# Optimization experiments

Measured on AMD Instinct MI355X. Metric: run time of the kernel, lower is better.

The kernel has to match this reference:

```python
import jax, jax.numpy as jnp
import numpy as np

HD, M = 4096, 14336

def setup_inputs() -> dict:
    key = jax.random.key(0)
    k_x, k_g, k_u, k_d = jax.random.split(key, 4)
    scale = 1.0 / np.sqrt(HD)
    x = jax.random.normal(k_x, (4, 2048, HD), dtype=jnp.float16)
    # Dequantized fp16 weights, stored torch-style as [out_features, in_features]
    W_gate = (jax.random.normal(k_g, (M, HD), dtype=jnp.float16) * jnp.float16(scale))
    W_up   = (jax.random.normal(k_u, (M, HD), dtype=jnp.float16) * jnp.float16(scale))
    W_down = (jax.random.normal(k_d, (HD, M), dtype=jnp.float16) * jnp.float16(1.0 / np.sqrt(M)))
    return {"x": x, "W_gate": W_gate, "W_up": W_up, "W_down": W_down}

def reference(x, W_gate, W_up, W_down):
    # SwiGLU: down( silu(x @ Wg^T) * (x @ Wu^T) )
    gate = jnp.einsum("bsh,mh->bsm", x, W_gate)   # [B,S,M]
    up = jnp.einsum("bsh,mh->bsm", x, W_up)       # [B,S,M]
    h = jax.nn.silu(gate) * up                       # fused elementwise
    out = jnp.einsum("bsm,hm->bsh", h, W_down)    # [B,S,HD]
    return out
```

## Files before the change

### kernel.cpp

```cpp
#include <hip/hip_runtime.h>

typedef _Float16 f16;
typedef _Float16 f16x8 __attribute__((ext_vector_type(8)));
typedef float f32x4 __attribute__((ext_vector_type(4)));

__device__ __forceinline__ f16x8 cvt8(f32x4 lo, f32x4 hi) {
    f16x8 h;
    h[0] = (f16)lo[0]; h[1] = (f16)lo[1]; h[2] = (f16)lo[2]; h[3] = (f16)lo[3];
    h[4] = (f16)hi[0]; h[5] = (f16)hi[1]; h[6] = (f16)hi[2]; h[7] = (f16)hi[3];
    return h;
}

__global__ __launch_bounds__(256)
void cvt_f32_f16(const float* __restrict__ in, f16* __restrict__ out, long long n) {
    long long i = ((long long)blockIdx.x * 256 + threadIdx.x) * 8;
    const long long stride = (long long)gridDim.x * 256 * 8;
    for (; i < n; i += stride) {
        f32x4 a = *(const f32x4*)(in + i);
        f32x4 b = *(const f32x4*)(in + i + 4);
        *(f16x8*)(out + i) = cvt8(a, b);
    }
}

__global__ void fill_sentinel_f32(float* __restrict__ out, long long n) {
    long long i = (long long)blockIdx.x * blockDim.x + threadIdx.x;
    long long stride = (long long)gridDim.x * blockDim.x;
    for (; i < n; i += stride) out[i] = 1.0f;
}

__device__ __forceinline__ void gload_lds16(const f16* g, f16* l) {
    __builtin_amdgcn_global_load_lds(
        (const __attribute__((address_space(1))) unsigned int*)(unsigned long long)g,
        (__attribute__((address_space(3))) unsigned int*)(unsigned int)(unsigned long long)l,
        16, 0, 0);
}

template<bool FUSED>
__global__ __launch_bounds__(512)
void mlp_gemm16(const f16* __restrict__ A, const f16* __restrict__ B0,
                const f16* __restrict__ B1, void* __restrict__ Cv,
                int K, int ldc, int nRow, int nCol, int RG) {
    constexpr int BN    = FUSED ? 128 : 256;
    constexpr int BROWS = FUSED ? 128 : 256;
    __shared__ __align__(16) f16 smA[3][128 * 32];
    __shared__ __align__(16) f16 smB0[3][BROWS * 32];
    __shared__ __align__(16) f16 smB1[FUSED ? 3 : 1][FUSED ? 128 * 32 : 8];

    const int lin   = blockIdx.x;
    const int perSg = RG * nCol;
    const int sg    = lin / perSg;
    const int rem   = lin - sg * perSg;
    int rgIn = nRow - sg * RG; if (rgIn > RG) rgIn = RG;
    const int colB = rem / rgIn;
    const int rowB = sg * RG + (rem - colB * rgIn);

    const long long blockRow = (long long)rowB * 128;
    const long long blockCol = (long long)colB * BN;

    const int tid  = threadIdx.x;
    const int w    = tid >> 6;
    const int lane = tid & 63;
    const int waveM = w >> 2;
    const int waveN = w & 3;

    const int dr   = tid >> 2;
    const int dblk = tid & 3;
    const int gblk = (dblk - (dr >> 1)) & 3;
    const f16* gA   = A  + (blockRow + dr) * (long long)K + gblk * 8;
    const f16* gB0a = B0 + (blockCol + dr) * (long long)K + gblk * 8;
    const f16* gB0b = FUSED ? nullptr
                            : B0 + (blockCol + 128 + dr) * (long long)K + gblk * 8;
    const f16* gB1a = FUSED ? B1 + (blockCol + dr) * (long long)K + gblk * 8
                            : nullptr;
    const int wbase = w * 512;

    const int fr = lane & 15;
    const int hi = lane >> 4;
    constexpr int NI = FUSED ? 2 : 4;
    int aOff[4], bOff[NI];
#pragma unroll
    for (int i = 0; i < 4; ++i) {
        const int r = waveM * 64 + i * 16 + fr;
        aOff[i] = r * 32 + (((hi + (r >> 1)) & 3) << 3);
    }
#pragma unroll
    for (int n = 0; n < NI; ++n) {
        const int r = waveN * (FUSED ? 32 : 64) + n * 16 + fr;
        bOff[n] = r * 32 + (((hi + (r >> 1)) & 3) << 3);
    }

    f32x4 acc0[4][NI];
    f32x4 acc1[FUSED ? 4 : 1][FUSED ? NI : 1];
#pragma unroll
    for (int mi = 0; mi < 4; ++mi)
#pragma unroll
        for (int ni = 0; ni < NI; ++ni) {
            acc0[mi][ni] = (f32x4){0.f, 0.f, 0.f, 0.f};
            if constexpr (FUSED) acc1[mi][ni] = (f32x4){0.f, 0.f, 0.f, 0.f};
        }

    auto stage = [&](int b) {
        gload_lds16(gA, &smA[b][wbase]);     gA += 32;
        gload_lds16(gB0a, &smB0[b][wbase]);  gB0a += 32;
        if constexpr (FUSED) {
            gload_lds16(gB1a, &smB1[b][wbase]); gB1a += 32;
        } else {
            gload_lds16(gB0b, &smB0[b][4096 + wbase]); gB0b += 32;
        }
    };

    auto compute = [&](int b) {
        f16x8 aF[4], bF[NI], b1F[FUSED ? NI : 1];
#pragma unroll
        for (int i = 0; i < 4; ++i) aF[i] = *(const f16x8*)(&smA[b][aOff[i]]);
#pragma unroll
        for (int n = 0; n < NI; ++n) bF[n] = *(const f16x8*)(&smB0[b][bOff[n]]);
        if constexpr (FUSED) {
#pragma unroll
            for (int n = 0; n < NI; ++n) b1F[n] = *(const f16x8*)(&smB1[b][bOff[n]]);
        }
#pragma unroll
        for (int mi = 0; mi < 4; ++mi)
#pragma unroll
            for (int ni = 0; ni < NI; ++ni) {
                acc0[mi][ni] = __builtin_amdgcn_mfma_f32_16x16x32_f16(
                    aF[mi], bF[ni], acc0[mi][ni], 0, 0, 0);
                if constexpr (FUSED)
                    acc1[mi][ni] = __builtin_amdgcn_mfma_f32_16x16x32_f16(
                        aF[mi], b1F[ni], acc1[mi][ni], 0, 0, 0);
            }
    };

    const int nk = K >> 5;
    stage(0);
    stage(1);
    int cur = 0;
    for (int t = 0; t < nk - 1; ++t) {
        asm volatile("s_waitcnt vmcnt(3)" ::: "memory");
        __builtin_amdgcn_s_barrier();
        __builtin_amdgcn_sched_barrier(0);
        if (t + 2 < nk) {
            int nb = cur + 2; if (nb >= 3) nb -= 3;
            stage(nb);
        }
        compute(cur);
        cur = (cur == 2) ? 0 : cur + 1;
    }
    asm volatile("s_waitcnt vmcnt(0)" ::: "memory");
    __builtin_amdgcn_s_barrier();
    __builtin_amdgcn_sched_barrier(0);
    compute(cur);

    const long long orBase = blockRow + waveM * 64 + hi * 4;
    const long long ocBase = blockCol + waveN * (FUSED ? 32 : 64) + fr;
#pragma unroll
    for (int mi = 0; mi < 4; ++mi)
#pragma unroll
        for (int ni = 0; ni < NI; ++ni)
#pragma unroll
            for (int j = 0; j < 4; ++j) {
                const long long idx =
                    (orBase + mi * 16 + j) * (long long)ldc + (ocBase + ni * 16);
                if constexpr (FUSED) {
                    float gv = acc0[mi][ni][j];
                    float uv = acc1[mi][ni][j];
                    float v = (gv / (1.f + __expf(-gv))) * uv;
                    ((f16*)Cv)[idx] = (f16)v;
                } else {
                    ((float*)Cv)[idx] = acc0[mi][ni][j];
                }
            }
}

template<bool IS16>
__device__ __forceinline__ f16x8 load8(const char* p) {
    if constexpr (IS16) return *(const f16x8*)p;
    const float* f = (const float*)p;
    return cvt8(*(const f32x4*)f, *(const f32x4*)(f + 4));
}

template<bool FUSED, bool A16, bool B16>
__global__ __launch_bounds__(256)
void mlp_gemm(const void* __restrict__ Av, const void* __restrict__ B0v,
              const void* __restrict__ B1v, void* __restrict__ Cv,
              int K, int ldc, int nRow, int nCol, int RG) {
    __shared__ __align__(16) f16 smA[128 * 32];
    __shared__ __align__(16) f16 smB0[128 * 32];
    __shared__ __align__(16) f16 smB1[FUSED ? 128 * 32 : 8];

    const int lin   = blockIdx.x;
    const int perSg = RG * nCol;
    const int sg    = lin / perSg;
    const int rem   = lin - sg * perSg;
    int rgIn = nRow - sg * RG; if (rgIn > RG) rgIn = RG;
    const int colB = rem / rgIn;
    const int rowB = sg * RG + (rem - colB * rgIn);

    const long long blockRow = (long long)rowB * 128;
    const long long blockCol = (long long)colB * 128;

    const int tid  = threadIdx.x;
    const int w    = tid >> 6;
    const int lane = tid & 63;
    const int waveM = w >> 1;
    const int waveN = w & 1;

    const int r0 = tid >> 2;
    const int s0 = tid & 3;
    const int szA = A16 ? 2 : 4;
    const int szB = B16 ? 2 : 4;
    const char* gA0  = (const char*)Av  + ((blockRow + r0)      * (long long)K + s0 * 8) * szA;
    const char* gA1  = (const char*)Av  + ((blockRow + r0 + 64) * (long long)K + s0 * 8) * szA;
    const char* gB00 = (const char*)B0v + ((blockCol + r0)      * (long long)K + s0 * 8) * szB;
    const char* gB01 = (const char*)B0v + ((blockCol + r0 + 64) * (long long)K + s0 * 8) * szB;
    const char* gB10 = FUSED ? (const char*)B1v + ((blockCol + r0)      * (long long)K + s0 * 8) * szB : nullptr;
    const char* gB11 = FUSED ? (const char*)B1v + ((blockCol + r0 + 64) * (long long)K + s0 * 8) * szB : nullptr;

    const int off0 = tid * 8;
    const int off1 = off0 + 2048;

    const int fr = lane & 15;
    const int fk = (lane >> 4) * 8;
    int offA[4], offB[4];
#pragma unroll
    for (int i = 0; i < 4; ++i) {
        offA[i] = (waveM * 64 + i * 16 + fr) * 32 + fk;
        offB[i] = (waveN * 64 + i * 16 + fr) * 32 + fk;
    }

    f32x4 acc0[4][4];
    f32x4 acc1[4][4];
#pragma unroll
    for (int mi = 0; mi < 4; ++mi)
#pragma unroll
        for (int ni = 0; ni < 4; ++ni) {
            acc0[mi][ni] = (f32x4){0.f, 0.f, 0.f, 0.f};
            if constexpr (FUSED) acc1[mi][ni] = (f32x4){0.f, 0.f, 0.f, 0.f};
        }

    const int ksteps = K >> 5;
    for (int kt = 0; kt < ksteps; ++kt) {
        f16x8 vA0  = load8<A16>(gA0);
        f16x8 vA1  = load8<A16>(gA1);
        f16x8 vB00 = load8<B16>(gB00);
        f16x8 vB01 = load8<B16>(gB01);
        f16x8 vB10, vB11;
        if constexpr (FUSED) {
            vB10 = load8<B16>(gB10);
            vB11 = load8<B16>(gB11);
        }
        gA0 += 32 * szA; gA1 += 32 * szA;
        gB00 += 32 * szB; gB01 += 32 * szB;
        if constexpr (FUSED) { gB10 += 32 * szB; gB11 += 32 * szB; }

        __syncthreads();

        *(f16x8*)(smA  + off0) = vA0;
        *(f16x8*)(smA  + off1) = vA1;
        *(f16x8*)(smB0 + off0) = vB00;
        *(f16x8*)(smB0 + off1) = vB01;
        if constexpr (FUSED) {
            *(f16x8*)(smB1 + off0) = vB10;
            *(f16x8*)(smB1 + off1) = vB11;
        }

        __syncthreads();

        f16x8 aF[4], bF[4], b1F[4];
#pragma unroll
        for (int i = 0; i < 4; ++i) aF[i] = *(const f16x8*)(smA + offA[i]);
#pragma unroll
        for (int i = 0; i < 4; ++i) bF[i] = *(const f16x8*)(smB0 + offB[i]);
        if constexpr (FUSED) {
#pragma unroll
            for (int i = 0; i < 4; ++i) b1F[i] = *(const f16x8*)(smB1 + offB[i]);
        }

#pragma unroll
        for (int mi = 0; mi < 4; ++mi)
#pragma unroll
            for (int ni = 0; ni < 4; ++ni) {
                acc0[mi][ni] = __builtin_amdgcn_mfma_f32_16x16x32_f16(
                    aF[mi], bF[ni], acc0[mi][ni], 0, 0, 0);
                if constexpr (FUSED)
                    acc1[mi][ni] = __builtin_amdgcn_mfma_f32_16x16x32_f16(
                        aF[mi], b1F[ni], acc1[mi][ni], 0, 0, 0);
            }
    }

    const long long orBase = blockRow + waveM * 64 + ((lane >> 4) * 4);
    const long long ocBase = blockCol + waveN * 64 + fr;
#pragma unroll
    for (int mi = 0; mi < 4; ++mi)
#pragma unroll
        for (int ni = 0; ni < 4; ++ni)
#pragma unroll
            for (int j = 0; j < 4; ++j) {
                const long long idx =
                    (orBase + mi * 16 + j) * (long long)ldc + (ocBase + ni * 16);
                if constexpr (FUSED) {
                    float gv = acc0[mi][ni][j];
                    float uv = acc1[mi][ni][j];
                    float v = (gv / (1.f + __expf(-gv))) * uv;
                    ((f16*)Cv)[idx] = (f16)v;
                } else {
                    ((float*)Cv)[idx] = acc0[mi][ni][j];
                }
            }
}

extern "C" void kernel_launch(void* const* d_in, const int* in_sizes, int n_in,
                              void* d_out, int out_size, void* d_ws, size_t ws_size,
                              hipStream_t stream) {
    const float* x  = (const float*)d_in[0];
    const float* Wg = (const float*)d_in[1];
    const float* Wu = (const float*)d_in[2];
    const float* Wd = (const float*)d_in[3];
    float* out = (float*)d_out;

    const int HD = 4096;
    const int T  = in_sizes[0] / HD;
    const int M  = in_sizes[1] / HD;

    const long long nW = (long long)M * HD;
    const long long nX = (long long)T * HD;
    const size_t wBytes = (size_t)nW * 2;
    const size_t xBytes = (size_t)nX * 2;
    const size_t hRow   = (size_t)M * 2;
    const size_t minH   = 128 * hRow;

    char* p = (char*)d_ws;
    size_t rem = ws_size;
    f16 *Wg16 = nullptr, *Wu16 = nullptr, *Wd16 = nullptr, *X16 = nullptr;
    bool wf16 = false, xf16 = false;
    if (rem >= 3 * wBytes + minH) {
        Wg16 = (f16*)p; p += wBytes;
        Wu16 = (f16*)p; p += wBytes;
        Wd16 = (f16*)p; p += wBytes;
        rem -= 3 * wBytes;
        wf16 = true;
        if (rem >= xBytes + minH) {
            X16 = (f16*)p; p += xBytes; rem -= xBytes; xf16 = true;
        }
    }
    f16* H = (f16*)p;
    long long maxRows = (long long)(rem / hRow);
    int chunk = (int)((maxRows / 128) * 128);
    if (chunk > T) chunk = T;
    if (chunk <= 0) {
        fill_sentinel_f32<<<1024, 256, 0, stream>>>(out, (long long)out_size);
        return;
    }

    if (wf16) {
        cvt_f32_f16<<<2048, 256, 0, stream>>>(Wg, Wg16, nW);
        cvt_f32_f16<<<2048, 256, 0, stream>>>(Wu, Wu16, nW);
        cvt_f32_f16<<<2048, 256, 0, stream>>>(Wd, Wd16, nW);
    }
    if (xf16) cvt_f32_f16<<<2048, 256, 0, stream>>>(x, X16, nX);

    for (int t0 = 0; t0 < T; t0 += chunk) {
        int rows = (T - t0 < chunk) ? (T - t0) : chunk;
        int nRow = rows / 128;
        {
            int nCol = M / 128;
            dim3 grid(nRow * nCol);
            int RG = nRow;
            if (xf16)
                mlp_gemm16<true><<<grid, 512, 0, stream>>>(
                    X16 + (size_t)t0 * HD, Wg16, Wu16, H, HD, M, nRow, nCol, RG);
            else if (wf16)
                mlp_gemm<true, false, true><<<grid, 256, 0, stream>>>(
                    x + (size_t)t0 * HD, Wg16, Wu16, H, HD, M, nRow, nCol, RG);
            else
                mlp_gemm<true, false, false><<<grid, 256, 0, stream>>>(
                    x + (size_t)t0 * HD, Wg, Wu, H, HD, M, nRow, nCol, RG);
        }
        {
            if (wf16) {
                int nCol = HD / 256;
                dim3 grid(nRow * nCol);
                int RG = (nRow < 32) ? nRow : 32;
                mlp_gemm16<false><<<grid, 512, 0, stream>>>(
                    H, Wd16, nullptr, out + (size_t)t0 * HD, M, HD, nRow, nCol, RG);
            } else {
                int nCol = HD / 128;
                dim3 grid(nRow * nCol);
                int RG = (nRow < 32) ? nRow : 32;
                mlp_gemm<false, true, false><<<grid, 256, 0, stream>>>(
                    H, Wd, nullptr, out + (size_t)t0 * HD, M, HD, nRow, nCol, RG);
            }
        }
    }
}
```

Before: 3.076 ms.

## Double GEMM block row tile to 256 for higher operand reuse

Both the fused gate/up GEMM and the down-projection GEMM now compute 256-row output tiles per block, with each wave covering 128 rows and holding twice as many MFMA accumulators. A extra A-load per stage feeds the larger LDS tile, and the wait count is adjusted accordingly. This aims to halve weight re-reads per output row and increase MFMA work per LDS load, at the cost of much higher register and LDS use that may reduce occupancy or cause spills. The host path is simplified so the fp16 route requires workspace for all converted tensors, otherwise falling back to the fp32 kernels.

```diff
diff --git a/kernel.cpp b/kernel.cpp
--- a/kernel.cpp
+++ b/kernel.cpp
@@ -36,14 +36,13 @@
 }
 
 template<bool FUSED>
-__global__ __launch_bounds__(512)
-void mlp_gemm16(const f16* __restrict__ A, const f16* __restrict__ B0,
-                const f16* __restrict__ B1, void* __restrict__ Cv,
-                int K, int ldc, int nRow, int nCol, int RG) {
-    constexpr int BN    = FUSED ? 128 : 256;
-    constexpr int BROWS = FUSED ? 128 : 256;
-    __shared__ __align__(16) f16 smA[3][128 * 32];
-    __shared__ __align__(16) f16 smB0[3][BROWS * 32];
+__global__ __launch_bounds__(512, 2)
+void mlp_gemm16b(const f16* __restrict__ A, const f16* __restrict__ B0,
+                 const f16* __restrict__ B1, void* __restrict__ Cv,
+                 int K, int ldc, int nRow, int nCol, int RG) {
+    constexpr int BN = FUSED ? 128 : 256;
+    __shared__ __align__(16) f16 smA[3][256 * 32];
+    __shared__ __align__(16) f16 smB0[3][BN * 32];
     __shared__ __align__(16) f16 smB1[FUSED ? 3 : 1][FUSED ? 128 * 32 : 8];
 
     const int lin   = blockIdx.x;
@@ -54,7 +53,7 @@
     const int colB = rem / rgIn;
     const int rowB = sg * RG + (rem - colB * rgIn);
 
-    const long long blockRow = (long long)rowB * 128;
+    const long long blockRow = (long long)rowB * 256;
     const long long blockCol = (long long)colB * BN;
 
     const int tid  = threadIdx.x;
@@ -66,10 +65,10 @@
     const int dr   = tid >> 2;
     const int dblk = tid & 3;
     const int gblk = (dblk - (dr >> 1)) & 3;
-    const f16* gA   = A  + (blockRow + dr) * (long long)K + gblk * 8;
+    const f16* gA0  = A + (blockRow + dr) * (long long)K + gblk * 8;
+    const f16* gA1  = gA0 + 128 * (long long)K;
     const f16* gB0a = B0 + (blockCol + dr) * (long long)K + gblk * 8;
-    const f16* gB0b = FUSED ? nullptr
-                            : B0 + (blockCol + 128 + dr) * (long long)K + gblk * 8;
+    const f16* gB0b = FUSED ? nullptr : gB0a + 128 * (long long)K;
     const f16* gB1a = FUSED ? B1 + (blockCol + dr) * (long long)K + gblk * 8
                             : nullptr;
     const int wbase = w * 512;
@@ -77,22 +76,23 @@
     const int fr = lane & 15;
     const int hi = lane >> 4;
     constexpr int NI = FUSED ? 2 : 4;
-    int aOff[4], bOff[NI];
-#pragma unroll
-    for (int i = 0; i < 4; ++i) {
-        const int r = waveM * 64 + i * 16 + fr;
+    constexpr int NW = FUSED ? 32 : 64;
+    int aOff[8], bOff[NI];
+#pragma unroll
+    for (int i = 0; i < 8; ++i) {
+        const int r = waveM * 128 + i * 16 + fr;
         aOff[i] = r * 32 + (((hi + (r >> 1)) & 3) << 3);
     }
 #pragma unroll
     for (int n = 0; n < NI; ++n) {
-        const int r = waveN * (FUSED ? 32 : 64) + n * 16 + fr;
+        const int r = waveN * NW + n * 16 + fr;
         bOff[n] = r * 32 + (((hi + (r >> 1)) & 3) << 3);
     }
 
-    f32x4 acc0[4][NI];
-    f32x4 acc1[FUSED ? 4 : 1][FUSED ? NI : 1];
-#pragma unroll
-    for (int mi = 0; mi < 4; ++mi)
+    f32x4 acc0[8][NI];
+    f32x4 acc1[FUSED ? 8 : 1][FUSED ? NI : 1];
+#pragma unroll
+    for (int mi = 0; mi < 8; ++mi)
 #pragma unroll
         for (int ni = 0; ni < NI; ++ni) {
             acc0[mi][ni] = (f32x4){0.f, 0.f, 0.f, 0.f};
@@ -100,19 +100,20 @@
         }
 
     auto stage = [&](int b) {
-        gload_lds16(gA, &smA[b][wbase]);     gA += 32;
-        gload_lds16(gB0a, &smB0[b][wbase]);  gB0a += 32;
-        if constexpr (FUSED) {
-            gload_lds16(gB1a, &smB1[b][wbase]); gB1a += 32;
+        gload_lds16(gA0, &smA[b][wbase]);           gA0 += 32;
+        gload_lds16(gA1, &smA[b][4096 + wbase]);    gA1 += 32;
+        gload_lds16(gB0a, &smB0[b][wbase]);         gB0a += 32;
+        if constexpr (FUSED) {
+            gload_lds16(gB1a, &smB1[b][wbase]);     gB1a += 32;
         } else {
             gload_lds16(gB0b, &smB0[b][4096 + wbase]); gB0b += 32;
         }
     };
 
     auto compute = [&](int b) {
-        f16x8 aF[4], bF[NI], b1F[FUSED ? NI : 1];
-#pragma unroll
-        for (int i = 0; i < 4; ++i) aF[i] = *(const f16x8*)(&smA[b][aOff[i]]);
+        f16x8 aF[8], bF[NI], b1F[FUSED ? NI : 1];
+#pragma unroll
+        for (int i = 0; i < 8; ++i) aF[i] = *(const f16x8*)(&smA[b][aOff[i]]);
 #pragma unroll
         for (int n = 0; n < NI; ++n) bF[n] = *(const f16x8*)(&smB0[b][bOff[n]]);
         if constexpr (FUSED) {
@@ -120,7 +121,7 @@
             for (int n = 0; n < NI; ++n) b1F[n] = *(const f16x8*)(&smB1[b][bOff[n]]);
         }
 #pragma unroll
-        for (int mi = 0; mi < 4; ++mi)
+        for (int mi = 0; mi < 8; ++mi)
 #pragma unroll
             for (int ni = 0; ni < NI; ++ni) {
                 acc0[mi][ni] = __builtin_amdgcn_mfma_f32_16x16x32_f16(
@@ -136,7 +137,7 @@
     stage(1);
     int cur = 0;
     for (int t = 0; t < nk - 1; ++t) {
-        asm volatile("s_waitcnt vmcnt(3)" ::: "memory");
+        asm volatile("s_waitcnt vmcnt(4)" ::: "memory");
         __builtin_amdgcn_s_barrier();
         __builtin_amdgcn_sched_barrier(0);
         if (t + 2 < nk) {
@@ -151,10 +152,10 @@
     __builtin_amdgcn_sched_barrier(0);
     compute(cur);
 
-    const long long orBase = blockRow + waveM * 64 + hi * 4;
-    const long long ocBase = blockCol + waveN * (FUSED ? 32 : 64) + fr;
-#pragma unroll
-    for (int mi = 0; mi < 4; ++mi)
+    const long long orBase = blockRow + waveM * 128 + hi * 4;
+    const long long ocBase = blockCol + waveN * NW + fr;
+#pragma unroll
+    for (int mi = 0; mi < 8; ++mi)
 #pragma unroll
         for (int ni = 0; ni < NI; ++ni)
 #pragma unroll
@@ -327,69 +328,72 @@
     const size_t wBytes = (size_t)nW * 2;
     const size_t xBytes = (size_t)nX * 2;
     const size_t hRow   = (size_t)M * 2;
-    const size_t minH   = 128 * hRow;
+    const size_t minH   = 256 * hRow;
 
     char* p = (char*)d_ws;
     size_t rem = ws_size;
     f16 *Wg16 = nullptr, *Wu16 = nullptr, *Wd16 = nullptr, *X16 = nullptr;
-    bool wf16 = false, xf16 = false;
-    if (rem >= 3 * wBytes + minH) {
+    bool fast = false;
+    if (rem >= 3 * wBytes + xBytes + minH) {
         Wg16 = (f16*)p; p += wBytes;
         Wu16 = (f16*)p; p += wBytes;
         Wd16 = (f16*)p; p += wBytes;
-        rem -= 3 * wBytes;
-        wf16 = true;
-        if (rem >= xBytes + minH) {
-            X16 = (f16*)p; p += xBytes; rem -= xBytes; xf16 = true;
-        }
+        X16  = (f16*)p; p += xBytes;
+        rem -= 3 * wBytes + xBytes;
+        fast = true;
     }
     f16* H = (f16*)p;
-    long long maxRows = (long long)(rem / hRow);
+
+    if (fast) {
+        long long maxRows = (long long)(rem / hRow);
+        int chunk = (int)((maxRows / 256) * 256);
+        if (chunk > T) chunk = T;
+
+        cvt_f32_f16<<<2048, 256, 0, stream>>>(Wg, Wg16, nW);
+        cvt_f32_f16<<<2048, 256, 0, stream>>>(Wu, Wu16, nW);
+        cvt_f32_f16<<<2048, 256, 0, stream>>>(Wd, Wd16, nW);
+        cvt_f32_f16<<<2048, 256, 0, stream>>>(x, X16, nX);
+
+        for (int t0 = 0; t0 < T; t0 += chunk) {
+            int rows = (T - t0 < chunk) ? (T - t0) : chunk;
+            int nRow = rows / 256;
+            {
+                int nCol = M / 128;
+                int RG = nRow;
+                mlp_gemm16b<true><<<dim3(nRow * nCol), 512, 0, stream>>>(
+                    X16 + (size_t)t0 * HD, Wg16, Wu16, H, HD, M, nRow, nCol, RG);
+            }
+            {
+                int nCol = HD / 256;
+                int RG = (nRow < 16) ? nRow : 16;
+                mlp_gemm16b<false><<<dim3(nRow * nCol), 512, 0, stream>>>(
+                    H, Wd16, nullptr, out + (size_t)t0 * HD, M, HD, nRow, nCol, RG);
+            }
+        }
+        return;
+    }
+
+    long long maxRows = (long long)(ws_size / hRow);
     int chunk = (int)((maxRows / 128) * 128);
     if (chunk > T) chunk = T;
     if (chunk <= 0) {
         fill_sentinel_f32<<<1024, 256, 0, stream>>>(out, (long long)out_size);
         return;
     }
-
-    if (wf16) {
-        cvt_f32_f16<<<2048, 256, 0, stream>>>(Wg, Wg16, nW);
-        cvt_f32_f16<<<2048, 256, 0, stream>>>(Wu, Wu16, nW);
-        cvt_f32_f16<<<2048, 256, 0, stream>>>(Wd, Wd16, nW);
-    }
-    if (xf16) cvt_f32_f16<<<2048, 256, 0, stream>>>(x, X16, nX);
-
+    f16* Hf = (f16*)d_ws;
     for (int t0 = 0; t0 < T; t0 += chunk) {
         int rows = (T - t0 < chunk) ? (T - t0) : chunk;
         int nRow = rows / 128;
         {
             int nCol = M / 128;
-            dim3 grid(nRow * nCol);
-            int RG = nRow;
-            if (xf16)
-                mlp_gemm16<true><<<grid, 512, 0, stream>>>(
-                    X16 + (size_t)t0 * HD, Wg16, Wu16, H, HD, M, nRow, nCol, RG);
-            else if (wf16)
-                mlp_gemm<true, false, true><<<grid, 256, 0, stream>>>(
-                    x + (size_t)t0 * HD, Wg16, Wu16, H, HD, M, nRow, nCol, RG);
-            else
-                mlp_gemm<true, false, false><<<grid, 256, 0, stream>>>(
-                    x + (size_t)t0 * HD, Wg, Wu, H, HD, M, nRow, nCol, RG);
+            mlp_gemm<true, false, false><<<dim3(nRow * nCol), 256, 0, stream>>>(
+                x + (size_t)t0 * HD, Wg, Wu, Hf, HD, M, nRow, nCol, nRow);
         }
         {
-            if (wf16) {
-                int nCol = HD / 256;
-                dim3 grid(nRow * nCol);
-                int RG = (nRow < 32) ? nRow : 32;
-                mlp_gemm16<false><<<grid, 512, 0, stream>>>(
-                    H, Wd16, nullptr, out + (size_t)t0 * HD, M, HD, nRow, nCol, RG);
-            } else {
-                int nCol = HD / 128;
-                dim3 grid(nRow * nCol);
-                int RG = (nRow < 32) ? nRow : 32;
-                mlp_gemm<false, true, false><<<grid, 256, 0, stream>>>(
-                    H, Wd, nullptr, out + (size_t)t0 * HD, M, HD, nRow, nCol, RG);
-            }
-        }
-    }
-}
+            int nCol = HD / 128;
+            int RG = (nRow < 32) ? nRow : 32;
+            mlp_gemm<false, true, false><<<dim3(nRow * nCol), 256, 0, stream>>>(
+                Hf, Wd, nullptr, out + (size_t)t0 * HD, M, HD, nRow, nCol, RG);
+        }
+    }
+}
```

Result: faster. 2.760 ms, median of 2 (-10.3%).
